# Performance work log

Measured on AMD Instinct MI355X. Metric: run time of the kernel, lower is better.

The kernel has to match this reference:

```python
import jax, jax.numpy as jnp
import numpy as np

N_NODES = 128   # input_series_dim (nodes per graph)
FEAT = 512      # input_series_length
HID = 512       # hidden_channels
OUT = 10        # output_dimension
BATCH = 512     # batch_size


def setup_inputs() -> dict:
    key = jax.random.key(0)
    ks = jax.random.split(key, 9)
    s = 0.02
    x = jax.random.normal(ks[0], (BATCH, N_NODES, FEAT), jnp.float32)
    # dense_to_sparse(ones(N_NODES, N_NODES)) -> fully connected incl. diagonal,
    # row-major order, covering only nodes 0..N_NODES-1 (faithful to source).
    r = jnp.repeat(jnp.arange(N_NODES, dtype=jnp.int32), N_NODES)
    c = jnp.tile(jnp.arange(N_NODES, dtype=jnp.int32), N_NODES)
    edge_index = jnp.stack([r, c])  # (2, N_NODES**2)
    batch = jnp.repeat(jnp.arange(BATCH, dtype=jnp.int32), N_NODES)  # (BATCH*N_NODES,)
    W1 = jax.random.normal(ks[1], (FEAT, HID), jnp.float32) * s
    b1 = jnp.zeros((HID,), jnp.float32)
    W2 = jax.random.normal(ks[2], (HID, HID), jnp.float32) * s
    b2 = jnp.zeros((HID,), jnp.float32)
    W3 = jax.random.normal(ks[3], (HID, HID), jnp.float32) * s
    b3 = jnp.zeros((HID,), jnp.float32)
    Wlin = jax.random.normal(ks[4], (HID, OUT), jnp.float32) * s
    blin = jnp.zeros((OUT,), jnp.float32)
    return {"x": x, "W1": W1, "b1": b1, "W2": W2, "b2": b2, "W3": W3,
            "b3": b3, "Wlin": Wlin, "blin": blin,
            "edge_index": edge_index, "batch": batch}


def gcn_conv(h, src, dst, W, b):
    # PyG GCNConv: linear transform, add self-loops for ALL N nodes, symmetric norm,
    # scatter-add aggregate at dst, add bias.
    N = h.shape[0]
    h = h @ W
    loop = jnp.arange(N, dtype=src.dtype)
    s = jnp.concatenate([src, loop])
    d = jnp.concatenate([dst, loop])
    deg = jax.ops.segment_sum(jnp.ones(s.shape[0], h.dtype), d, num_segments=N)
    dinv = jnp.where(deg > 0, jax.lax.rsqrt(deg), jnp.zeros((), h.dtype))
    norm = dinv[s] * dinv[d]                     # (E+N,)
    out = jax.ops.segment_sum(norm[:, None] * h[s], d, num_segments=N)
    return out + b


def reference(x, W1, b1, W2, b2, W3, b3, Wlin, blin, edge_index, batch):
    x = x.reshape(-1, x.shape[-1]).astype(jnp.float32)   # (B*N_NODES, FEAT)
    src, dst = edge_index[0], edge_index[1]
    h = jax.nn.relu(gcn_conv(x, src, dst, W1, b1))
    h = jax.nn.relu(gcn_conv(h, src, dst, W2, b2))
    h = gcn_conv(h, src, dst, W3, b3)                    # layers == 3 path
    B = BATCH
    sums = jax.ops.segment_sum(h, batch, num_segments=B)
    cnt = jax.ops.segment_sum(jnp.ones((h.shape[0],), h.dtype), batch, num_segments=B)
    pooled = sums / cnt[:, None]                         # global_mean_pool
    # dropout p=0.5 is identity in eval mode
    return pooled @ Wlin + blin                          # (BATCH, OUT)
```

## Files before the change

kernel.cpp:

```cpp
#include <hip/hip_runtime.h>
#include <hip/hip_bf16.h>


typedef __attribute__((ext_vector_type(8))) short short8;
typedef __attribute__((ext_vector_type(4))) float f32x4;
typedef __attribute__((ext_vector_type(2))) unsigned int uint2v;
typedef __attribute__((ext_vector_type(4))) unsigned int uint4v;

#define AS_G __attribute__((address_space(1)))
#define AS_L __attribute__((address_space(3)))

__device__ __forceinline__ void gload_lds16(const void* g, void* l) {
  __builtin_amdgcn_global_load_lds((const AS_G void*)g, (AS_L void*)l, 16, 0, 0);
}

#define FENCE_BARRIER()                      \
  do {                                       \
    asm volatile("" ::: "memory");           \
    __builtin_amdgcn_s_barrier();            \
    asm volatile("" ::: "memory");           \
  } while (0)

__device__ __forceinline__ unsigned int pack2_bf16(float a, float b) {
  unsigned int ua = __float_as_uint(a);
  unsigned int ub = __float_as_uint(b);
  ua += 0x7FFFu + ((ua >> 16) & 1u);
  ub += 0x7FFFu + ((ub >> 16) & 1u);
  return (ua >> 16) | (ub & 0xFFFF0000u);
}

__device__ __forceinline__ unsigned short bf16_rne(float a) {
  unsigned int ua = __float_as_uint(a);
  ua += 0x7FFFu + ((ua >> 16) & 1u);
  return (unsigned short)(ua >> 16);
}

__global__ __launch_bounds__(512, 4) void gemm1(
    const float* __restrict__ x,
    const __hip_bfloat16* __restrict__ W1t,
    const float* __restrict__ b1,
    unsigned short* __restrict__ H1)
{
  __shared__ __align__(16) __hip_bfloat16 smem[38400];

  const int t    = threadIdx.x;
  const int orig = blockIdx.x;
  const int wgid = (orig & 7) * 128 + (orig >> 3);
  const int g    = wgid >> 1;
  const int nb   = wgid & 1;

  const int wave = t >> 6;
  const int l    = t & 63;
  const int q    = l >> 4;
  const int r16  = l & 15;
  const int wm   = (wave & 1) * 64;
  const int wn   = (wave >> 1) * 64;

  const int arow = t >> 2;
  const int slot = t & 3;
  const int achk = slot ^ ((arow >> 1) & 3);
  const float* gx = x + (size_t)(g * 128 + arow) * 512 + achk * 8;

  const int nrow0 = t >> 2;
  const int nrow1 = 128 + (t >> 2);
  const __hip_bfloat16* gb0 = W1t + (size_t)(nb * 256 + nrow0) * 512 +
                              ((slot ^ ((nrow0 >> 1) & 3)) << 3);
  const __hip_bfloat16* gb1 = W1t + (size_t)(nb * 256 + nrow1) * 512 +
                              ((slot ^ ((nrow1 >> 1) & 3)) << 3);

  f32x4 acc[4][4];
#pragma unroll
  for (int i = 0; i < 4; ++i)
#pragma unroll
    for (int j = 0; j < 4; ++j)
      acc[i][j] = (f32x4)0.0f;

  int u0 = 0, u1 = 12288, u2 = 24576;

  f32x4 pA0, pA1;
  pA0 = *(const f32x4*)(const void*)gx;
  pA1 = *(const f32x4*)(const void*)(gx + 4);
  gload_lds16(gb0, smem + u0 + 4096 + wave * 512);
  gload_lds16(gb1, smem + u0 + 8192 + wave * 512);
  {
    uint4v w;
    w[0] = pack2_bf16(pA0[0], pA0[1]);
    w[1] = pack2_bf16(pA0[2], pA0[3]);
    w[2] = pack2_bf16(pA1[0], pA1[1]);
    w[3] = pack2_bf16(pA1[2], pA1[3]);
    *(uint4v*)(void*)(smem + u0 + t * 8) = w;
  }
  pA0 = *(const f32x4*)(const void*)(gx + 32);
  pA1 = *(const f32x4*)(const void*)(gx + 36);
  gload_lds16(gb0 + 32, smem + u1 + 4096 + wave * 512);
  gload_lds16(gb1 + 32, smem + u1 + 8192 + wave * 512);
  asm volatile("s_waitcnt vmcnt(4)" ::: "memory");
  asm volatile("s_waitcnt lgkmcnt(0)" ::: "memory");
  FENCE_BARRIER();

  for (int kt = 0; kt < 16; ++kt) {
    if (kt < 15) {
      uint4v w;
      w[0] = pack2_bf16(pA0[0], pA0[1]);
      w[1] = pack2_bf16(pA0[2], pA0[3]);
      w[2] = pack2_bf16(pA1[0], pA1[1]);
      w[3] = pack2_bf16(pA1[2], pA1[3]);
      *(uint4v*)(void*)(smem + u1 + t * 8) = w;
    }
    if (kt < 14) {
      const int ko = (kt + 2) * 32;
      pA0 = *(const f32x4*)(const void*)(gx + ko);
      pA1 = *(const f32x4*)(const void*)(gx + ko + 4);
      gload_lds16(gb0 + ko, smem + u2 + 4096 + wave * 512);
      gload_lds16(gb1 + ko, smem + u2 + 8192 + wave * 512);
      asm volatile("s_waitcnt vmcnt(4)" ::: "memory");
    } else {
      asm volatile("s_waitcnt vmcnt(0)" ::: "memory");
    }
    short8 af[4], bfr[4];
#pragma unroll
    for (int i = 0; i < 4; ++i) {
      const int row = wm + i * 16 + r16;
      const int c   = (q ^ ((row >> 1) & 3)) << 3;
      af[i] = *(const short8*)(const void*)(smem + u0 + row * 32 + c);
    }
#pragma unroll
    for (int j = 0; j < 4; ++j) {
      const int row = wn + j * 16 + r16;
      const int c   = (q ^ ((row >> 1) & 3)) << 3;
      bfr[j] = *(const short8*)(const void*)(smem + u0 + 4096 + row * 32 + c);
    }
    __builtin_amdgcn_s_setprio(1);
#pragma unroll
    for (int i = 0; i < 4; ++i)
#pragma unroll
      for (int j = 0; j < 4; ++j)
        acc[i][j] = __builtin_amdgcn_mfma_f32_16x16x32_bf16(af[i], bfr[j], acc[i][j], 0, 0, 0);
    __builtin_amdgcn_s_setprio(0);

    if (kt < 15) {
      asm volatile("s_waitcnt lgkmcnt(0)" ::: "memory");
      FENCE_BARRIER();
    }
    const int tmp = u0; u0 = u1; u1 = u2; u2 = tmp;
  }
  __syncthreads();

  float* redf = (float*)(smem + 36864);
  float* Sbuf = (float*)(smem + 37888);
  const size_t hbase = (size_t)g * 128 * 512 + nb * 256;

  if (g == 0) {
    float sj[4];
#pragma unroll
    for (int j = 0; j < 4; ++j) {
      float a = 0.0f;
#pragma unroll
      for (int i = 0; i < 4; ++i)
#pragma unroll
        for (int r = 0; r < 4; ++r)
          a += acc[i][j][r];
      a += __shfl_xor(a, 16, 64);
      a += __shfl_xor(a, 32, 64);
      sj[j] = a;
    }
    __syncthreads();
    if (q == 0) {
#pragma unroll
      for (int j = 0; j < 4; ++j) redf[wave * 64 + j * 16 + r16] = sj[j];
    }
    __syncthreads();
    if (t < 256)
      Sbuf[t] = redf[(2 * (t >> 6)) * 64 + (t & 63)] +
                redf[(2 * (t >> 6) + 1) * 64 + (t & 63)];
    __syncthreads();
    float bvv[4], Svv[4];
#pragma unroll
    for (int j = 0; j < 4; ++j) {
      bvv[j] = b1[nb * 256 + wn + j * 16 + r16];
      Svv[j] = Sbuf[wn + j * 16 + r16];
    }
#pragma unroll
    for (int i = 0; i < 4; ++i)
#pragma unroll
      for (int r = 0; r < 4; ++r) {
        const int row = wm + i * 16 + q * 4 + r;
#pragma unroll
        for (int j = 0; j < 4; ++j) {
          const float v = fmaxf((Svv[j] + acc[i][j][r]) * (1.0f / 129.0f) + bvv[j], 0.0f);
          const float o = __shfl_xor(v, 1, 64);
          if ((r16 & 1) == 0)
            *(unsigned int*)(void*)(H1 + hbase + (size_t)row * 512 + wn + j * 16 + r16) =
                pack2_bf16(v, o);
        }
      }
  } else {
    float bvv[4];
#pragma unroll
    for (int j = 0; j < 4; ++j) bvv[j] = b1[nb * 256 + wn + j * 16 + r16];
#pragma unroll
    for (int i = 0; i < 4; ++i)
#pragma unroll
      for (int r = 0; r < 4; ++r) {
        const int row = wm + i * 16 + q * 4 + r;
#pragma unroll
        for (int j = 0; j < 4; ++j) {
          const float v = fmaxf(acc[i][j][r] + bvv[j], 0.0f);
          const float o = __shfl_xor(v, 1, 64);
          if ((r16 & 1) == 0)
            *(unsigned int*)(void*)(H1 + hbase + (size_t)row * 512 + wn + j * 16 + r16) =
                pack2_bf16(v, o);
        }
      }
  }
}

__global__ __launch_bounds__(512, 4) void gemm2(
    const unsigned short* __restrict__ H1,
    const __hip_bfloat16* __restrict__ W2t,
    const float* __restrict__ b2,
    float* __restrict__ P)
{
  __shared__ __align__(16) __hip_bfloat16 smem[38400];

  const int t    = threadIdx.x;
  const int orig = blockIdx.x;
  const int wgid = (orig & 7) * 128 + (orig >> 3);
  const int g    = wgid >> 1;
  const int nb   = wgid & 1;

  const int wave = t >> 6;
  const int l    = t & 63;
  const int q    = l >> 4;
  const int r16  = l & 15;
  const int wm   = (wave & 1) * 64;
  const int wn   = (wave >> 1) * 64;

  const int arow = t >> 2;
  const int slot = t & 3;
  const unsigned short* gaA = H1 + (size_t)(g * 128 + arow) * 512 +
                              ((slot ^ ((arow >> 1) & 3)) << 3);
  const int nrow0 = t >> 2;
  const int nrow1 = 128 + (t >> 2);
  const __hip_bfloat16* gb0 = W2t + (size_t)(nb * 256 + nrow0) * 512 +
                              ((slot ^ ((nrow0 >> 1) & 3)) << 3);
  const __hip_bfloat16* gb1 = W2t + (size_t)(nb * 256 + nrow1) * 512 +
                              ((slot ^ ((nrow1 >> 1) & 3)) << 3);

  f32x4 acc[4][4];
#pragma unroll
  for (int i = 0; i < 4; ++i)
#pragma unroll
    for (int j = 0; j < 4; ++j)
      acc[i][j] = (f32x4)0.0f;

  int u0 = 0, u1 = 12288, u2 = 24576;

  gload_lds16(gaA,      smem + u0 + wave * 512);
  gload_lds16(gb0,      smem + u0 + 4096 + wave * 512);
  gload_lds16(gb1,      smem + u0 + 8192 + wave * 512);
  gload_lds16(gaA + 32, smem + u1 + wave * 512);
  gload_lds16(gb0 + 32, smem + u1 + 4096 + wave * 512);
  gload_lds16(gb1 + 32, smem + u1 + 8192 + wave * 512);
  asm volatile("s_waitcnt vmcnt(3)" ::: "memory");
  FENCE_BARRIER();

  for (int kt = 0; kt < 16; ++kt) {
    if (kt < 14) {
      const int ko = (kt + 2) * 32;
      gload_lds16(gaA + ko, smem + u2 + wave * 512);
      gload_lds16(gb0 + ko, smem + u2 + 4096 + wave * 512);
      gload_lds16(gb1 + ko, smem + u2 + 8192 + wave * 512);
      asm volatile("s_waitcnt vmcnt(3)" ::: "memory");
    } else {
      asm volatile("s_waitcnt vmcnt(0)" ::: "memory");
    }
    short8 af[4], bfr[4];
#pragma unroll
    for (int i = 0; i < 4; ++i) {
      const int row = wm + i * 16 + r16;
      const int c   = (q ^ ((row >> 1) & 3)) << 3;
      af[i] = *(const short8*)(const void*)(smem + u0 + row * 32 + c);
    }
#pragma unroll
    for (int j = 0; j < 4; ++j) {
      const int row = wn + j * 16 + r16;
      const int c   = (q ^ ((row >> 1) & 3)) << 3;
      bfr[j] = *(const short8*)(const void*)(smem + u0 + 4096 + row * 32 + c);
    }
    __builtin_amdgcn_s_setprio(1);
#pragma unroll
    for (int i = 0; i < 4; ++i)
#pragma unroll
      for (int j = 0; j < 4; ++j)
        acc[i][j] = __builtin_amdgcn_mfma_f32_16x16x32_bf16(af[i], bfr[j], acc[i][j], 0, 0, 0);
    __builtin_amdgcn_s_setprio(0);

    if (kt < 15) {
      asm volatile("s_waitcnt lgkmcnt(0)" ::: "memory");
      FENCE_BARRIER();
    }
    const int tmp = u0; u0 = u1; u1 = u2; u2 = tmp;
  }
  __syncthreads();

  float* redf = (float*)(smem + 36864);
  float* Sbuf = (float*)(smem + 37888);

  float pj[4];
  if (g == 0) {
    float sj[4];
#pragma unroll
    for (int j = 0; j < 4; ++j) {
      float a = 0.0f;
#pragma unroll
      for (int i = 0; i < 4; ++i)
#pragma unroll
        for (int r = 0; r < 4; ++r)
          a += acc[i][j][r];
      a += __shfl_xor(a, 16, 64);
      a += __shfl_xor(a, 32, 64);
      sj[j] = a;
    }
    __syncthreads();
    if (q == 0) {
#pragma unroll
      for (int j = 0; j < 4; ++j) redf[wave * 64 + j * 16 + r16] = sj[j];
    }
    __syncthreads();
    if (t < 256)
      Sbuf[t] = redf[(2 * (t >> 6)) * 64 + (t & 63)] +
                redf[(2 * (t >> 6) + 1) * 64 + (t & 63)];
    __syncthreads();
#pragma unroll
    for (int j = 0; j < 4; ++j) {
      const int col = wn + j * 16 + r16;
      const float bv = b2[nb * 256 + col];
      const float Sv = Sbuf[col];
      float a = 0.0f;
#pragma unroll
      for (int i = 0; i < 4; ++i)
#pragma unroll
        for (int r = 0; r < 4; ++r)
          a += fmaxf((Sv + acc[i][j][r]) * (1.0f / 129.0f) + bv, 0.0f);
      a += __shfl_xor(a, 16, 64);
      a += __shfl_xor(a, 32, 64);
      pj[j] = a;
    }
    __syncthreads();
  } else {
#pragma unroll
    for (int j = 0; j < 4; ++j) {
      const float bv = b2[nb * 256 + wn + j * 16 + r16];
      float a = 0.0f;
#pragma unroll
      for (int i = 0; i < 4; ++i)
#pragma unroll
        for (int r = 0; r < 4; ++r)
          a += fmaxf(acc[i][j][r] + bv, 0.0f);
      a += __shfl_xor(a, 16, 64);
      a += __shfl_xor(a, 32, 64);
      pj[j] = a;
    }
    __syncthreads();
  }
  if (q == 0) {
#pragma unroll
    for (int j = 0; j < 4; ++j) redf[wave * 64 + j * 16 + r16] = pj[j];
  }
  __syncthreads();
  if (t < 256)
    P[(size_t)g * 512 + nb * 256 + t] =
        (redf[(2 * (t >> 6)) * 64 + (t & 63)] +
         redf[(2 * (t >> 6) + 1) * 64 + (t & 63)]) * (1.0f / 128.0f);
}

__global__ void final_out(const float* __restrict__ P,
                          const float* __restrict__ Wf,
                          const float* __restrict__ bfv,
                          float* __restrict__ out) {
  const int m = blockIdx.x;
  const int l = threadIdx.x;
  float acc[10];
#pragma unroll
  for (int o = 0; o < 10; ++o) acc[o] = 0.0f;
  for (int c = l; c < 512; c += 64) {
    const float p = P[m * 512 + c];
#pragma unroll
    for (int o = 0; o < 10; ++o) acc[o] += p * Wf[c * 10 + o];
  }
#pragma unroll
  for (int off = 32; off; off >>= 1)
#pragma unroll
    for (int o = 0; o < 10; ++o) acc[o] += __shfl_down(acc[o], off, 64);
  if (l == 0) {
#pragma unroll
    for (int o = 0; o < 10; ++o) out[m * 10 + o] = acc[o] + bfv[o];
  }
}

__global__ __launch_bounds__(1024) void fused_gcn(
    const float* __restrict__ x,
    const __hip_bfloat16* __restrict__ W1t,
    const __hip_bfloat16* __restrict__ W2t,
    const float* __restrict__ b1,
    const float* __restrict__ b2,
    const float* __restrict__ Wf,
    const float* __restrict__ bfv,
    float* __restrict__ out)
{
  __shared__ __align__(16) __hip_bfloat16 smem[81920];

  const int t  = threadIdx.x;
  const int g  = blockIdx.x;
  const int wave = t >> 6;
  const int l    = t & 63;
  const int q    = l >> 4;
  const int r16  = l & 15;
  const int wm   = (wave & 1) * 64;
  const int wn   = (wave >> 1) * 64;

  const int arow = t >> 3;
  const int kq   = t & 7;
  const float* ga = x + ((size_t)g * 128 + arow) * 512 + kq * 4;
  const int awoff = arow * 32 + (((kq >> 1) ^ ((arow >> 1) & 3)) << 3) + (kq & 1) * 4;

  const int brow = t >> 2;
  const int bgc  = (t & 3) ^ ((brow >> 1) & 3);
  const size_t boff = (size_t)brow * 512 + bgc * 8;
  const __hip_bfloat16* g1b0 = W1t + boff;
  const __hip_bfloat16* g1b1 = g1b0 + (size_t)256 * 512;

  f32x4 acc[4][4];
#pragma unroll
  for (int i = 0; i < 4; ++i)
#pragma unroll
    for (int j = 0; j < 4; ++j)
      acc[i][j] = (f32x4)0.0f;

  {
    f32x4 a0 = *(const f32x4*)(const void*)ga;
    gload_lds16(g1b0, smem + 49152 + wave * 512);
    gload_lds16(g1b1, smem + 49152 + 8192 + wave * 512);
    uint2v w;
    w[0] = pack2_bf16(a0[0], a0[1]);
    w[1] = pack2_bf16(a0[2], a0[3]);
    *(uint2v*)(void*)(smem + awoff) = w;
  }
  for (int kt = 0; kt < 16; ++kt) {
    const int cur = kt & 1;
    const int nxt = cur ^ 1;
    __syncthreads();

    f32x4 aN;
    if (kt < 15) {
      const int ko = (kt + 1) * 32;
      aN = *(const f32x4*)(const void*)(ga + ko);
      gload_lds16(g1b0 + ko, smem + 49152 + nxt * 16384 + wave * 512);
      gload_lds16(g1b1 + ko, smem + 49152 + nxt * 16384 + 8192 + wave * 512);
    }

    short8 af[4], bfr[4];
#pragma unroll
    for (int i = 0; i < 4; ++i) {
      const int row = wm + i * 16 + r16;
      const int c   = (q ^ ((row >> 1) & 3)) << 3;
      af[i] = *(const short8*)(const void*)(smem + cur * 4096 + row * 32 + c);
    }
#pragma unroll
    for (int j = 0; j < 4; ++j) {
      const int row = wn + j * 16 + r16;
      const int c   = (q ^ ((row >> 1) & 3)) << 3;
      bfr[j] = *(const short8*)(const void*)(smem + 49152 + cur * 16384 + row * 32 + c);
    }
#pragma unroll
    for (int i = 0; i < 4; ++i)
#pragma unroll
      for (int j = 0; j < 4; ++j)
        acc[i][j] = __builtin_amdgcn_mfma_f32_16x16x32_bf16(af[i], bfr[j], acc[i][j], 0, 0, 0);

    if (kt < 15) {
      uint2v w;
      w[0] = pack2_bf16(aN[0], aN[1]);
      w[1] = pack2_bf16(aN[2], aN[3]);
      *(uint2v*)(void*)(smem + nxt * 4096 + awoff) = w;
    }
  }
  __syncthreads();

  const __hip_bfloat16* g2b0 = W2t + boff;
  const __hip_bfloat16* g2b1 = g2b0 + (size_t)256 * 512;
  gload_lds16(g2b0, smem + 65536 + wave * 512);

  float* redf = (float*)(smem + 73728);
  float* Sbuf = (float*)(smem + 75776);

  if (g == 0) {
    float sj[4];
#pragma unroll
    for (int j = 0; j < 4; ++j) {
      float a = 0.0f;
#pragma unroll
      for (int i = 0; i < 4; ++i)
#pragma unroll
        for (int r = 0; r < 4; ++r)
          a += acc[i][j][r];
      a += __shfl_xor(a, 16, 64);
      a += __shfl_xor(a, 32, 64);
      sj[j] = a;
    }
    if (q == 0) {
#pragma unroll
      for (int j = 0; j < 4; ++j) redf[wave * 64 + j * 16 + r16] = sj[j];
    }
    __syncthreads();
    if (t < 512)
      Sbuf[t] = redf[((t >> 6) * 2) * 64 + (t & 63)] +
                redf[((t >> 6) * 2 + 1) * 64 + (t & 63)];
    __syncthreads();
#pragma unroll
    for (int j = 0; j < 4; ++j) {
      const int col = wn + j * 16 + r16;
      const float bv = b1[col];
      const float Sv = Sbuf[col];
#pragma unroll
      for (int i = 0; i < 4; ++i)
#pragma unroll
        for (int r = 0; r < 4; ++r) {
          const int row = wm + i * 16 + q * 4 + r;
          const float v = fmaxf((Sv + acc[i][j][r]) * (1.0f / 129.0f) + bv, 0.0f);
          const float o = __shfl_xor(v, 1, 64);
          if ((r16 & 1) == 0) {
            const int sl = (col >> 3) ^ (row & 7);
            *(unsigned int*)(void*)(smem + row * 512 + sl * 8 + (col & 7)) = pack2_bf16(v, o);
          }
        }
    }
  } else {
#pragma unroll
    for (int j = 0; j < 4; ++j) {
      const int col = wn + j * 16 + r16;
      const float bv = b1[col];
#pragma unroll
      for (int i = 0; i < 4; ++i)
#pragma unroll
        for (int r = 0; r < 4; ++r) {
          const int row = wm + i * 16 + q * 4 + r;
          const float v = fmaxf(acc[i][j][r] + bv, 0.0f);
          const float o = __shfl_xor(v, 1, 64);
          if ((r16 & 1) == 0) {
            const int sl = (col >> 3) ^ (row & 7);
            *(unsigned int*)(void*)(smem + row * 512 + sl * 8 + (col & 7)) = pack2_bf16(v, o);
          }
        }
    }
  }

#pragma unroll
  for (int i = 0; i < 4; ++i)
#pragma unroll
    for (int j = 0; j < 4; ++j)
      acc[i][j] = (f32x4)0.0f;

  for (int kt = 0; kt < 16; ++kt) {
    __syncthreads();
    gload_lds16(g2b1 + kt * 32, smem + 73728 + wave * 512);
    if (wave < 8) {
      short8 af[4], bfr[4];
#pragma unroll
      for (int i = 0; i < 4; ++i) {
        const int row = wm + i * 16 + r16;
        const int sl  = (kt * 4 + q) ^ (row & 7);
        af[i] = *(const short8*)(const void*)(smem + row * 512 + sl * 8);
      }
#pragma unroll
      for (int j = 0; j < 4; ++j) {
        const int row = wn + j * 16 + r16;
        const int c   = (q ^ ((row >> 1) & 3)) << 3;
        bfr[j] = *(const short8*)(const void*)(smem + 65536 + row * 32 + c);
      }
      __builtin_amdgcn_s_setprio(1);
#pragma unroll
      for (int i = 0; i < 4; ++i)
#pragma unroll
        for (int j = 0; j < 4; ++j)
          acc[i][j] = __builtin_amdgcn_mfma_f32_16x16x32_bf16(af[i], bfr[j], acc[i][j], 0, 0, 0);
      __builtin_amdgcn_s_setprio(0);
    }
    __syncthreads();
    if (kt < 15)
      gload_lds16(g2b0 + (kt + 1) * 32, smem + 65536 + wave * 512);
    if (wave >= 8) {
      short8 af[4], bfr[4];
#pragma unroll
      for (int i = 0; i < 4; ++i) {
        const int row = wm + i * 16 + r16;
        const int sl  = (kt * 4 + q) ^ (row & 7);
        af[i] = *(const short8*)(const void*)(smem + row * 512 + sl * 8);
      }
#pragma unroll
      for (int j = 0; j < 4; ++j) {
        const int row = wn + j * 16 + r16;
        const int c   = (q ^ ((row >> 1) & 3)) << 3;
        bfr[j] = *(const short8*)(const void*)(smem + 65536 + row * 32 + c);
      }
      __builtin_amdgcn_s_setprio(1);
#pragma unroll
      for (int i = 0; i < 4; ++i)
#pragma unroll
        for (int j = 0; j < 4; ++j)
          acc[i][j] = __builtin_amdgcn_mfma_f32_16x16x32_bf16(af[i], bfr[j], acc[i][j], 0, 0, 0);
      __builtin_amdgcn_s_setprio(0);
    }
  }
  __syncthreads();

  float pj[4];
  if (g == 0) {
    float sj[4];
#pragma unroll
    for (int j = 0; j < 4; ++j) {
      float a = 0.0f;
#pragma unroll
      for (int i = 0; i < 4; ++i)
#pragma unroll
        for (int r = 0; r < 4; ++r)
          a += acc[i][j][r];
      a += __shfl_xor(a, 16, 64);
      a += __shfl_xor(a, 32, 64);
      sj[j] = a;
    }
    if (q == 0) {
#pragma unroll
      for (int j = 0; j < 4; ++j) redf[wave * 64 + j * 16 + r16] = sj[j];
    }
    __syncthreads();
    if (t < 512)
      Sbuf[t] = redf[((t >> 6) * 2) * 64 + (t & 63)] +
                redf[((t >> 6) * 2 + 1) * 64 + (t & 63)];
    __syncthreads();
#pragma unroll
    for (int j = 0; j < 4; ++j) {
      const float bv = b2[wn + j * 16 + r16];
      const float Sv = Sbuf[wn + j * 16 + r16];
      float a = 0.0f;
#pragma unroll
      for (int i = 0; i < 4; ++i)
#pragma unroll
        for (int r = 0; r < 4; ++r)
          a += fmaxf((Sv + acc[i][j][r]) * (1.0f / 129.0f) + bv, 0.0f);
      a += __shfl_xor(a, 16, 64);
      a += __shfl_xor(a, 32, 64);
      pj[j] = a;
    }
  } else {
#pragma unroll
    for (int j = 0; j < 4; ++j) {
      const float bv = b2[wn + j * 16 + r16];
      float a = 0.0f;
#pragma unroll
      for (int i = 0; i < 4; ++i)
#pragma unroll
        for (int r = 0; r < 4; ++r)
          a += fmaxf(acc[i][j][r] + bv, 0.0f);
      a += __shfl_xor(a, 16, 64);
      a += __shfl_xor(a, 32, 64);
      pj[j] = a;
    }
  }
  if (q == 0) {
#pragma unroll
    for (int j = 0; j < 4; ++j) redf[wave * 64 + j * 16 + r16] = pj[j];
  }
  __syncthreads();
  if (t < 512)
    Sbuf[t] =
        (redf[((t >> 6) * 2) * 64 + (t & 63)] +
         redf[((t >> 6) * 2 + 1) * 64 + (t & 63)]) * (1.0f / 128.0f);
  __syncthreads();

  if (wave < 10) {
    float s = 0.0f;
    for (int c = l; c < 512; c += 64) s += Sbuf[c] * Wf[c * 10 + wave];
#pragma unroll
    for (int off = 32; off; off >>= 1) s += __shfl_down(s, off, 64);
    if (l == 0) out[(size_t)g * 10 + wave] = s + bfv[wave];
  }
}

__global__ __launch_bounds__(1024) void prep(
    const float* __restrict__ W1, const float* __restrict__ W2,
    unsigned short* __restrict__ W1t, unsigned short* __restrict__ W2t,
    const float* __restrict__ W3, const float* __restrict__ Wlin,
    const float* __restrict__ b3, const float* __restrict__ blin,
    float* __restrict__ Wf, float* __restrict__ bfv) {
  const int b = blockIdx.x;
  if (b < 512) {
    __shared__ float tile[32][33];
    const int z  = b >> 8;
    const int by = (b >> 4) & 15;
    const int bx = b & 15;
    const float* W = z ? W2 : W1;
    unsigned short* Wt = z ? W2t : W1t;
    const int tx = threadIdx.x & 31;
    const int ty = threadIdx.x >> 5;
    tile[ty][tx] = W[(by * 32 + ty) * 512 + bx * 32 + tx];
    __syncthreads();
    Wt[(bx * 32 + ty) * 512 + by * 32 + tx] = bf16_rne(tile[tx][ty]);
  } else {
    const int c = b - 512;
    const int l = threadIdx.x;
    if (l < 64) {
      float acc[10];
#pragma unroll
      for (int o = 0; o < 10; ++o) acc[o] = 0.0f;
      for (int n = l; n < 512; n += 64) {
        const float wv = W3[c * 512 + n];
#pragma unroll
        for (int o = 0; o < 10; ++o) acc[o] += wv * Wlin[n * 10 + o];
      }
#pragma unroll
      for (int off = 32; off; off >>= 1)
#pragma unroll
        for (int o = 0; o < 10; ++o) acc[o] += __shfl_down(acc[o], off, 64);
      if (l == 0) {
#pragma unroll
        for (int o = 0; o < 10; ++o) Wf[c * 10 + o] = acc[o];
      }
      if (c < 10) {
        float s = 0.0f;
        for (int k = l; k < 512; k += 64) s += b3[k] * Wlin[k * 10 + c];
#pragma unroll
        for (int off = 32; off; off >>= 1) s += __shfl_down(s, off, 64);
        if (l == 0) bfv[c] = s + blin[c];
      }
    }
  }
}

extern "C" void kernel_launch(void* const* d_in, const int* in_sizes, int n_in,
                              void* d_out, int out_size, void* d_ws, size_t ws_size,
                              hipStream_t stream) {
  const float* x    = (const float*)d_in[0];
  const float* W1   = (const float*)d_in[1];
  const float* b1   = (const float*)d_in[2];
  const float* W2   = (const float*)d_in[3];
  const float* b2   = (const float*)d_in[4];
  const float* W3   = (const float*)d_in[5];
  const float* b3   = (const float*)d_in[6];
  const float* Wlin = (const float*)d_in[7];
  const float* blin = (const float*)d_in[8];
  float* out = (float*)d_out;

  char* ws = (char*)d_ws;
  unsigned short* W1t = (unsigned short*)ws;
  unsigned short* W2t = W1t + 512 * 512;
  float* Wf           = (float*)(W2t + 512 * 512);
  float* bfv          = Wf + 512 * 10;
  float* P            = bfv + 16;
  unsigned short* H1  = (unsigned short*)(P + 512 * 512);

  const size_t need = (size_t)512 * 512 * 2 * 2 +
                      (512 * 10 + 16 + 512 * 512) * 4 +
                      (size_t)65536 * 512 * 2;

  const bool split = ws_size >= need;

  prep<<<1024, 1024, 0, stream>>>(
      W1, W2, W1t, W2t, W3, Wlin, b3, blin, Wf, bfv);

  if (split) {
    gemm1<<<1024, 512, 0, stream>>>(x, (const __hip_bfloat16*)W1t, b1, H1);
    gemm2<<<1024, 512, 0, stream>>>(H1, (const __hip_bfloat16*)W2t, b2, P);
    final_out<<<512, 64, 0, stream>>>(P, Wf, bfv, out);
  } else {
    fused_gcn<<<512, 1024, 0, stream>>>(
        x, (const __hip_bfloat16*)W1t, (const __hip_bfloat16*)W2t, b1, b2, Wf, bfv, out);
  }
}
```

Before: 294.3 us.

## Stream fp32 A tiles directly into LDS and convert to bf16 at fragment load

In gemm1, the fp32 x tiles no longer go through registers with a bf16 pack and an LDS store. They are loaded straight into LDS with global_load_lds as fp32, using a 3-stage ring and an XOR swizzle, and converted to bf16 when the MFMA fragments are read. The B tiles now use a separate double buffer, and the waits switch from lgkmcnt to vmcnt counting. This removes register staging and LDS write instructions from the A path, but doubles the LDS footprint and bandwidth for A and adds conversion work inside the inner loop. The larger shared allocation may also reduce occupancy.

```diff
diff --git a/kernel.cpp b/kernel.cpp
--- a/kernel.cpp
+++ b/kernel.cpp
@@ -5,7 +5,6 @@
 typedef __attribute__((ext_vector_type(8))) short short8;
 typedef __attribute__((ext_vector_type(4))) float f32x4;
 typedef __attribute__((ext_vector_type(2))) unsigned int uint2v;
-typedef __attribute__((ext_vector_type(4))) unsigned int uint4v;
 
 #define AS_G __attribute__((address_space(1)))
 #define AS_L __attribute__((address_space(3)))
@@ -41,7 +40,7 @@
     const float* __restrict__ b1,
     unsigned short* __restrict__ H1)
 {
-  __shared__ __align__(16) __hip_bfloat16 smem[38400];
+  __shared__ __align__(16) __hip_bfloat16 smem[40960];
 
   const int t    = threadIdx.x;
   const int orig = blockIdx.x;
@@ -56,11 +55,11 @@
   const int wm   = (wave & 1) * 64;
   const int wn   = (wave >> 1) * 64;
 
-  const int arow = t >> 2;
-  const int slot = t & 3;
-  const int achk = slot ^ ((arow >> 1) & 3);
-  const float* gx = x + (size_t)(g * 128 + arow) * 512 + achk * 8;
-
+  const int axor = (t & 7) ^ ((t >> 3) & 7);
+  const float* gx0 = x + (size_t)(g * 128 + (t >> 3)) * 512 + axor * 4;
+  const float* gx1 = x + (size_t)(g * 128 + 64 + (t >> 3)) * 512 + axor * 4;
+
+  const int slot  = t & 3;
   const int nrow0 = t >> 2;
   const int nrow1 = 128 + (t >> 2);
   const __hip_bfloat16* gb0 = W1t + (size_t)(nb * 256 + nrow0) * 512 +
@@ -75,60 +74,54 @@
     for (int j = 0; j < 4; ++j)
       acc[i][j] = (f32x4)0.0f;
 
-  int u0 = 0, u1 = 12288, u2 = 24576;
-
-  f32x4 pA0, pA1;
-  pA0 = *(const f32x4*)(const void*)gx;
-  pA1 = *(const f32x4*)(const void*)(gx + 4);
-  gload_lds16(gb0, smem + u0 + 4096 + wave * 512);
-  gload_lds16(gb1, smem + u0 + 8192 + wave * 512);
-  {
-    uint4v w;
-    w[0] = pack2_bf16(pA0[0], pA0[1]);
-    w[1] = pack2_bf16(pA0[2], pA0[3]);
-    w[2] = pack2_bf16(pA1[0], pA1[1]);
-    w[3] = pack2_bf16(pA1[2], pA1[3]);
-    *(uint4v*)(void*)(smem + u0 + t * 8) = w;
-  }
-  pA0 = *(const f32x4*)(const void*)(gx + 32);
-  pA1 = *(const f32x4*)(const void*)(gx + 36);
-  gload_lds16(gb0 + 32, smem + u1 + 4096 + wave * 512);
-  gload_lds16(gb1 + 32, smem + u1 + 8192 + wave * 512);
-  asm volatile("s_waitcnt vmcnt(4)" ::: "memory");
-  asm volatile("s_waitcnt lgkmcnt(0)" ::: "memory");
+  gload_lds16(gx0, smem + wave * 512);
+  gload_lds16(gx1, smem + 4096 + wave * 512);
+  gload_lds16(gb0, smem + 24576 + wave * 512);
+  gload_lds16(gb1, smem + 24576 + 4096 + wave * 512);
+  gload_lds16(gx0 + 32, smem + 8192 + wave * 512);
+  gload_lds16(gx1 + 32, smem + 8192 + 4096 + wave * 512);
+  asm volatile("s_waitcnt vmcnt(2)" ::: "memory");
   FENCE_BARRIER();
 
+  const char* smemb = (const char*)smem;
+
   for (int kt = 0; kt < 16; ++kt) {
+    const int As = kt % 3;
     if (kt < 15) {
-      uint4v w;
-      w[0] = pack2_bf16(pA0[0], pA0[1]);
-      w[1] = pack2_bf16(pA0[2], pA0[3]);
-      w[2] = pack2_bf16(pA1[0], pA1[1]);
-      w[3] = pack2_bf16(pA1[2], pA1[3]);
-      *(uint4v*)(void*)(smem + u1 + t * 8) = w;
+      const int ko = (kt + 1) * 32;
+      const int bs = 24576 + ((kt + 1) & 1) * 8192;
+      gload_lds16(gb0 + ko, smem + bs + wave * 512);
+      gload_lds16(gb1 + ko, smem + bs + 4096 + wave * 512);
     }
     if (kt < 14) {
       const int ko = (kt + 2) * 32;
-      pA0 = *(const f32x4*)(const void*)(gx + ko);
-      pA1 = *(const f32x4*)(const void*)(gx + ko + 4);
-      gload_lds16(gb0 + ko, smem + u2 + 4096 + wave * 512);
-      gload_lds16(gb1 + ko, smem + u2 + 8192 + wave * 512);
-      asm volatile("s_waitcnt vmcnt(4)" ::: "memory");
-    } else {
-      asm volatile("s_waitcnt vmcnt(0)" ::: "memory");
-    }
+      const int as2 = ((kt + 2) % 3) * 8192;
+      gload_lds16(gx0 + ko, smem + as2 + wave * 512);
+      gload_lds16(gx1 + ko, smem + as2 + 4096 + wave * 512);
+    }
+
     short8 af[4], bfr[4];
 #pragma unroll
     for (int i = 0; i < 4; ++i) {
       const int row = wm + i * 16 + r16;
-      const int c   = (q ^ ((row >> 1) & 3)) << 3;
-      af[i] = *(const short8*)(const void*)(smem + u0 + row * 32 + c);
+      const int s0  = (q * 2) ^ (row & 7);
+      const f32x4 v0 = *(const f32x4*)(const void*)(smemb + As * 16384 + row * 128 + s0 * 16);
+      const f32x4 v1 = *(const f32x4*)(const void*)(smemb + As * 16384 + row * 128 + (s0 ^ 1) * 16);
+      uint2v w0, w1;
+      w0[0] = pack2_bf16(v0[0], v0[1]);
+      w0[1] = pack2_bf16(v0[2], v0[3]);
+      w1[0] = pack2_bf16(v1[0], v1[1]);
+      w1[1] = pack2_bf16(v1[2], v1[3]);
+      union { uint2v u[2]; short8 s; } cvt;
+      cvt.u[0] = w0;
+      cvt.u[1] = w1;
+      af[i] = cvt.s;
     }
 #pragma unroll
     for (int j = 0; j < 4; ++j) {
       const int row = wn + j * 16 + r16;
       const int c   = (q ^ ((row >> 1) & 3)) << 3;
-      bfr[j] = *(const short8*)(const void*)(smem + u0 + 4096 + row * 32 + c);
+      bfr[j] = *(const short8*)(const void*)(smem + 24576 + (kt & 1) * 8192 + row * 32 + c);
     }
     __builtin_amdgcn_s_setprio(1);
 #pragma unroll
@@ -139,15 +132,17 @@
     __builtin_amdgcn_s_setprio(0);
 
     if (kt < 15) {
-      asm volatile("s_waitcnt lgkmcnt(0)" ::: "memory");
+      if (kt < 14)
+        asm volatile("s_waitcnt vmcnt(2)" ::: "memory");
+      else
+        asm volatile("s_waitcnt vmcnt(0)" ::: "memory");
       FENCE_BARRIER();
     }
-    const int tmp = u0; u0 = u1; u1 = u2; u2 = tmp;
   }
   __syncthreads();
 
-  float* redf = (float*)(smem + 36864);
-  float* Sbuf = (float*)(smem + 37888);
+  float* redf = (float*)(smem);
+  float* Sbuf = (float*)(smem + 1024);
   const size_t hbase = (size_t)g * 128 * 512 + nb * 256;
 
   if (g == 0) {
```

New measurement: 297.2 us. No clear change (+1.0%).

## Pre-convert x to bf16 in prep and stream A tiles via direct LDS loads

Applied to the files above, without the earlier changes.

Moves the fp32-to-bf16 conversion of the input activations out of gemm1 into the prep kernel, writing a bf16 copy of x to workspace. gemm1 then loads A tiles with asynchronous global-to-LDS loads like the B tiles, removing register staging and pack work in the main loop. This adds an extra pass over x (read fp32, write bf16) and enlarges the workspace requirement, which could force the fused fallback if the workspace is too small.

```diff
diff --git a/kernel.cpp b/kernel.cpp
--- a/kernel.cpp
+++ b/kernel.cpp
@@ -5,7 +5,6 @@
 typedef __attribute__((ext_vector_type(8))) short short8;
 typedef __attribute__((ext_vector_type(4))) float f32x4;
 typedef __attribute__((ext_vector_type(2))) unsigned int uint2v;
-typedef __attribute__((ext_vector_type(4))) unsigned int uint4v;
 
 #define AS_G __attribute__((address_space(1)))
 #define AS_L __attribute__((address_space(3)))
@@ -36,7 +35,7 @@
 }
 
 __global__ __launch_bounds__(512, 4) void gemm1(
-    const float* __restrict__ x,
+    const unsigned short* __restrict__ xb,
     const __hip_bfloat16* __restrict__ W1t,
     const float* __restrict__ b1,
     unsigned short* __restrict__ H1)
@@ -58,9 +57,8 @@
 
   const int arow = t >> 2;
   const int slot = t & 3;
-  const int achk = slot ^ ((arow >> 1) & 3);
-  const float* gx = x + (size_t)(g * 128 + arow) * 512 + achk * 8;
-
+  const unsigned short* gaA = xb + (size_t)(g * 128 + arow) * 512 +
+                              ((slot ^ ((arow >> 1) & 3)) << 3);
   const int nrow0 = t >> 2;
   const int nrow1 = 128 + (t >> 2);
   const __hip_bfloat16* gb0 = W1t + (size_t)(nb * 256 + nrow0) * 512 +
@@ -77,43 +75,22 @@
 
   int u0 = 0, u1 = 12288, u2 = 24576;
 
-  f32x4 pA0, pA1;
-  pA0 = *(const f32x4*)(const void*)gx;
-  pA1 = *(const f32x4*)(const void*)(gx + 4);
-  gload_lds16(gb0, smem + u0 + 4096 + wave * 512);
-  gload_lds16(gb1, smem + u0 + 8192 + wave * 512);
-  {
-    uint4v w;
-    w[0] = pack2_bf16(pA0[0], pA0[1]);
-    w[1] = pack2_bf16(pA0[2], pA0[3]);
-    w[2] = pack2_bf16(pA1[0], pA1[1]);
-    w[3] = pack2_bf16(pA1[2], pA1[3]);
-    *(uint4v*)(void*)(smem + u0 + t * 8) = w;
-  }
-  pA0 = *(const f32x4*)(const void*)(gx + 32);
-  pA1 = *(const f32x4*)(const void*)(gx + 36);
+  gload_lds16(gaA,      smem + u0 + wave * 512);
+  gload_lds16(gb0,      smem + u0 + 4096 + wave * 512);
+  gload_lds16(gb1,      smem + u0 + 8192 + wave * 512);
+  gload_lds16(gaA + 32, smem + u1 + wave * 512);
   gload_lds16(gb0 + 32, smem + u1 + 4096 + wave * 512);
   gload_lds16(gb1 + 32, smem + u1 + 8192 + wave * 512);
-  asm volatile("s_waitcnt vmcnt(4)" ::: "memory");
-  asm volatile("s_waitcnt lgkmcnt(0)" ::: "memory");
+  asm volatile("s_waitcnt vmcnt(3)" ::: "memory");
   FENCE_BARRIER();
 
   for (int kt = 0; kt < 16; ++kt) {
-    if (kt < 15) {
-      uint4v w;
-      w[0] = pack2_bf16(pA0[0], pA0[1]);
-      w[1] = pack2_bf16(pA0[2], pA0[3]);
-      w[2] = pack2_bf16(pA1[0], pA1[1]);
-      w[3] = pack2_bf16(pA1[2], pA1[3]);
-      *(uint4v*)(void*)(smem + u1 + t * 8) = w;
-    }
     if (kt < 14) {
       const int ko = (kt + 2) * 32;
-      pA0 = *(const f32x4*)(const void*)(gx + ko);
-      pA1 = *(const f32x4*)(const void*)(gx + ko + 4);
+      gload_lds16(gaA + ko, smem + u2 + wave * 512);
       gload_lds16(gb0 + ko, smem + u2 + 4096 + wave * 512);
       gload_lds16(gb1 + ko, smem + u2 + 8192 + wave * 512);
-      asm volatile("s_waitcnt vmcnt(4)" ::: "memory");
+      asm volatile("s_waitcnt vmcnt(3)" ::: "memory");
     } else {
       asm volatile("s_waitcnt vmcnt(0)" ::: "memory");
     }
@@ -693,7 +670,8 @@
     unsigned short* __restrict__ W1t, unsigned short* __restrict__ W2t,
     const float* __restrict__ W3, const float* __restrict__ Wlin,
     const float* __restrict__ b3, const float* __restrict__ blin,
-    float* __restrict__ Wf, float* __restrict__ bfv) {
+    float* __restrict__ Wf, float* __restrict__ bfv,
+    const float* __restrict__ x, unsigned short* __restrict__ xb) {
   const int b = blockIdx.x;
   if (b < 512) {
     __shared__ float tile[32][33];
@@ -707,7 +685,7 @@
     tile[ty][tx] = W[(by * 32 + ty) * 512 + bx * 32 + tx];
     __syncthreads();
     Wt[(bx * 32 + ty) * 512 + by * 32 + tx] = bf16_rne(tile[tx][ty]);
-  } else {
+  } else if (b < 1024) {
     const int c = b - 512;
     const int l = threadIdx.x;
     if (l < 64) {
@@ -734,6 +712,18 @@
         for (int off = 32; off; off >>= 1) s += __shfl_down(s, off, 64);
         if (l == 0) bfv[c] = s + blin[c];
       }
+    }
+  } else {
+    const size_t base = (size_t)(b - 1024) * 8192;
+    const int tt = threadIdx.x;
+#pragma unroll
+    for (int jj = 0; jj < 2; ++jj) {
+      const size_t off = base + (size_t)jj * 4096 + (size_t)tt * 4;
+      const f32x4 v = *(const f32x4*)(const void*)(x + off);
+      uint2v w;
+      w[0] = pack2_bf16(v[0], v[1]);
+      w[1] = pack2_bf16(v[2], v[3]);
+      *(uint2v*)(void*)(xb + off) = w;
     }
   }
 }
@@ -759,18 +749,19 @@
   float* bfv          = Wf + 512 * 10;
   float* P            = bfv + 16;
   unsigned short* H1  = (unsigned short*)(P + 512 * 512);
+  unsigned short* xb  = H1 + (size_t)65536 * 512;
 
   const size_t need = (size_t)512 * 512 * 2 * 2 +
                       (512 * 10 + 16 + 512 * 512) * 4 +
-                      (size_t)65536 * 512 * 2;
+                      (size_t)65536 * 512 * 2 * 2;
 
   const bool split = ws_size >= need;
 
-  prep<<<1024, 1024, 0, stream>>>(
-      W1, W2, W1t, W2t, W3, Wlin, b3, blin, Wf, bfv);
+  prep<<<split ? 5120 : 1024, 1024, 0, stream>>>(
+      W1, W2, W1t, W2t, W3, Wlin, b3, blin, Wf, bfv, x, xb);
 
   if (split) {
-    gemm1<<<1024, 512, 0, stream>>>(x, (const __hip_bfloat16*)W1t, b1, H1);
+    gemm1<<<1024, 512, 0, stream>>>(xb, (const __hip_bfloat16*)W1t, b1, H1);
     gemm2<<<1024, 512, 0, stream>>>(H1, (const __hip_bfloat16*)W2t, b2, P);
     final_out<<<512, 64, 0, stream>>>(P, Wf, bfv, out);
   } else {
```

Measured after the change: 301.5 us. 1.02x slower.
